# Kernel tuning notes

Measured on AMD Instinct MI355X. Metric: run time of the kernel, lower is better.

The kernel has to match this reference:

```python
import jax, jax.numpy as jnp
import numpy as np

L = 43          # number of classes
C = L + 3       # <eps>, 'O', 'I-', + L class symbols
B = 128
T = 4096
NEG = jnp.float32(-1e30)


def setup_inputs() -> dict:
    key = jax.random.key(0)
    k1, k2, k3, k4 = jax.random.split(key, 4)
    logits = jax.random.normal(k1, (B, T, C), dtype=jnp.float32)
    log_probs = jax.nn.log_softmax(logits, axis=-1)
    input_lens = jax.random.randint(k2, (B,), T // 2, T + 1).astype(jnp.int32)
    labels = jax.random.randint(k3, (B, T), 1, C).astype(jnp.int32)  # valid (non-eps) symbols
    # den_scores parameter: one raw score per denominator arc (2L+4 arcs).
    # Layout: [0]=0->0 'O', [1:L+1]=0->0 labels, [L+1]=0->1 'I-', [L+2]=0->final,
    #         [L+3]=1->1 'I-', [L+4:2L+4]=1->0 labels.
    den_params = 0.01 * jax.random.normal(k4, (2 * L + 4,), dtype=jnp.float32)
    return {"log_probs": log_probs, "den_params": den_params,
            "input_lens": input_lens, "labels": labels}


def reference(log_probs, den_params, input_lens, labels):
    Bb, Tt, Cc = log_probs.shape
    Ll = Cc - 3
    # set_scores_stochastic_: per-source-state log-softmax of arc scores
    g0 = jax.nn.log_softmax(den_params[: Ll + 3])   # state-0 outgoing arcs
    g1 = jax.nn.log_softmax(den_params[Ll + 3:])    # state-1 outgoing arcs
    s_O, s0_lab, s_0I, s_fin = g0[0], g0[1:Ll + 1], g0[Ll + 1], g0[Ll + 2]
    s_1I, s1_lab = g1[0], g1[1:]

    mask = jnp.arange(Tt)[None, :] < input_lens[:, None]          # [B,T]

    # ---- numerator: linear FSA intersected with emissions = path score ----
    tok_lp = jnp.take_along_axis(log_probs, labels[..., None], axis=-1)[..., 0]
    num = jnp.sum(jnp.where(mask, tok_lp, 0.0), axis=1)           # [B]

    # ---- denominator: log-semiring forward DP over the 2-state topology ----
    lp_t = jnp.moveaxis(log_probs, 1, 0)    # [T,B,C]
    mask_t = jnp.moveaxis(mask, 1, 0)       # [T,B]

    def step(alpha, inputs):
        lp, m = inputs                       # lp [B,C], m [B]
        a0, a1 = alpha[:, 0], alpha[:, 1]
        lp_lab = lp[:, 3:]                   # emissions for class symbols, [B,L]
        # into state 0: 0->0 on 'O', 0->0 on each label, 1->0 on each label
        terms0 = jnp.concatenate([
            (a0 + s_O + lp[:, 1])[:, None],
            a0[:, None] + s0_lab[None, :] + lp_lab,
            a1[:, None] + s1_lab[None, :] + lp_lab,
        ], axis=1)
        n0 = jax.scipy.special.logsumexp(terms0, axis=1)
        # into state 1: 0->1 and 1->1, both on 'I-'
        terms1 = jnp.stack([a0 + s_0I + lp[:, 2], a1 + s_1I + lp[:, 2]], axis=1)
        n1 = jax.scipy.special.logsumexp(terms1, axis=1)
        new = jnp.stack([n0, n1], axis=1)
        new = jnp.where(m[:, None], new, alpha)  # frozen past each seq's length
        return new, None

    alpha0 = jnp.concatenate(
        [jnp.zeros((Bb, 1), log_probs.dtype), jnp.full((Bb, 1), NEG, log_probs.dtype)], axis=1)
    alpha, _ = jax.lax.scan(step, alpha0, (lp_t, mask_t))
    den = alpha[:, 0] + s_fin                                    # final arc 0->2 on -1

    return jnp.sum(num - den)
```

## Files before the change

kernel.cpp:

```cpp
#include <hip/hip_runtime.h>

#define BB 128
#define TT 4096
#define LL 43
#define CC 46
#define CHUNK 256
#define NC (TT / CHUNK)
#define TPB 256
#define NEGF (-1e30f)
#define L2E 1.44269504088896340736f
#define LN2 0.69314718055994530942f

__device__ __forceinline__ float la2(float x, float y) {
    float mx = fmaxf(x, y), mn = fminf(x, y);
    return mx + log2f(1.0f + exp2f(mn - mx));
}

__global__ void crf_prep(const float* __restrict__ dp, float* __restrict__ cst) {
    int lane = threadIdx.x;
    float x0 = (lane < CC) ? dp[lane] : NEGF;
    float x1 = (lane < LL + 1) ? dp[CC + lane] : NEGF;
    float mx0 = x0, mx1 = x1;
    #pragma unroll
    for (int m = 1; m < 64; m <<= 1) {
        mx0 = fmaxf(mx0, __shfl_xor(mx0, m));
        mx1 = fmaxf(mx1, __shfl_xor(mx1, m));
    }
    float e0 = (lane < CC) ? expf(x0 - mx0) : 0.0f;
    float e1 = (lane < LL + 1) ? expf(x1 - mx1) : 0.0f;
    float s0 = e0, s1 = e1;
    #pragma unroll
    for (int m = 1; m < 64; m <<= 1) {
        s0 += __shfl_xor(s0, m);
        s1 += __shfl_xor(s1, m);
    }
    float g0 = x0 - mx0 - logf(s0);
    float g1 = x1 - mx1 - logf(s1);
    if (lane >= 1 && lane <= LL) {
        cst[lane - 1] = expf(g0);
        cst[LL + lane - 1] = expf(g1);
    }
    if (lane == 0) { cst[86] = expf(g0); cst[88] = g1 * L2E; }
    if (lane == LL + 1) cst[87] = g0 * L2E;
    if (lane == LL + 2) cst[89] = g0 * L2E;
}

__global__ __launch_bounds__(TPB) void crf_chunk(
    const float* __restrict__ lp, const int* __restrict__ lens,
    const int* __restrict__ labels, const float* __restrict__ cst,
    float* __restrict__ res) {
    int b = blockIdx.y, c = blockIdx.x;
    int t0 = c * CHUNK;
    int len = lens[b];
    float* r = res + (b * NC + c) * 8;
    if (t0 >= len) {
        if (threadIdx.x == 0) { r[0] = 0.f; r[1] = NEGF; r[2] = NEGF; r[3] = 0.f; r[4] = 0.f; }
        return;
    }
    __shared__ float tile[CHUNK * CC];
    __shared__ float wres[TPB / 64][5];
    const float4* src = (const float4*)(lp + (size_t)(b * TT + t0) * CC);
    float4* dst = (float4*)tile;
    #pragma unroll 4
    for (int i = threadIdx.x; i < CHUNK * CC / 4; i += TPB) dst[i] = src[i];
    __syncthreads();

    int tid = threadIdx.x;
    int t = t0 + tid;
    const float* vr = tile + tid * CC;
    float m00, m01, m10, m11, tok;
    {
        float w1 = exp2f(L2E * vr[1]);
        float v2s = L2E * vr[2];
        float dot0 = cst[2 * LL] * w1;
        float dot1 = 0.f;
        #pragma unroll
        for (int j = 0; j < LL; ++j) {
            float w = exp2f(L2E * vr[3 + j]);
            dot0 = fmaf(cst[j], w, dot0);
            dot1 = fmaf(cst[LL + j], w, dot1);
        }
        m00 = log2f(dot0);
        m01 = log2f(dot1);
        m10 = cst[87] + v2s;
        m11 = cst[88] + v2s;
        int lab = labels[b * TT + t];
        tok = vr[lab];
    }
    if (t >= len) { m00 = 0.f; m01 = NEGF; m10 = NEGF; m11 = 0.f; tok = 0.f; }

    int lane = tid & 63;
    #pragma unroll
    for (int m = 1; m < 64; m <<= 1) {
        float p00 = __shfl_xor(m00, m), p01 = __shfl_xor(m01, m);
        float p10 = __shfl_xor(m10, m), p11 = __shfl_xor(m11, m);
        bool up = (lane & m) != 0;
        float a00 = up ? m00 : p00, a01 = up ? m01 : p01;
        float a10 = up ? m10 : p10, a11 = up ? m11 : p11;
        float b00 = up ? p00 : m00, b01 = up ? p01 : m01;
        float b10 = up ? p10 : m10, b11 = up ? p11 : m11;
        m00 = la2(a00 + b00, a01 + b10);
        m01 = la2(a00 + b01, a01 + b11);
        m10 = la2(a10 + b00, a11 + b10);
        m11 = la2(a10 + b01, a11 + b11);
        tok += __shfl_xor(tok, m);
    }
    if (lane == 0) {
        int w = tid >> 6;
        wres[w][0] = m00; wres[w][1] = m01; wres[w][2] = m10; wres[w][3] = m11; wres[w][4] = tok;
    }
    __syncthreads();
    if (tid == 0) {
        float c00 = wres[0][0], c01 = wres[0][1], c10 = wres[0][2], c11 = wres[0][3];
        float num = wres[0][4];
        #pragma unroll
        for (int w = 1; w < TPB / 64; ++w) {
            float a00 = wres[w][0], a01 = wres[w][1], a10 = wres[w][2], a11 = wres[w][3];
            float n00 = la2(a00 + c00, a01 + c10);
            float n01 = la2(a00 + c01, a01 + c11);
            float n10 = la2(a10 + c00, a11 + c10);
            float n11 = la2(a10 + c01, a11 + c11);
            c00 = n00; c01 = n01; c10 = n10; c11 = n11;
            num += wres[w][4];
        }
        r[0] = c00; r[1] = c01; r[2] = c10; r[3] = c11; r[4] = num;
    }
}

__global__ void crf_final(const float* __restrict__ cst, const float* __restrict__ res,
                          float* __restrict__ out) {
    int b = threadIdx.x;
    float a0 = 0.f, a1 = NEGF, num = 0.f;
    #pragma unroll
    for (int c = 0; c < NC; ++c) {
        const float* r = res + (b * NC + c) * 8;
        float n0 = la2(r[0] + a0, r[1] + a1);
        float n1 = la2(r[2] + a0, r[3] + a1);
        a0 = n0; a1 = n1; num += r[4];
    }
    float den = (a0 + cst[89]) * LN2;
    float val = num - den;
    #pragma unroll
    for (int m = 1; m < 64; m <<= 1) val += __shfl_xor(val, m);
    __shared__ float part[2];
    if ((b & 63) == 0) part[b >> 6] = val;
    __syncthreads();
    if (b == 0) out[0] = part[0] + part[1];
}

extern "C" void kernel_launch(void* const* d_in, const int* in_sizes, int n_in,
                              void* d_out, int out_size, void* d_ws, size_t ws_size,
                              hipStream_t stream) {
    const float* lp = (const float*)d_in[0];
    const float* dp = (const float*)d_in[1];
    const int* lens = (const int*)d_in[2];
    const int* labels = (const int*)d_in[3];
    float* out = (float*)d_out;
    float* cst = (float*)d_ws;
    float* res = cst + 96;

    hipLaunchKernelGGL(crf_prep, dim3(1), dim3(64), 0, stream, dp, cst);
    hipLaunchKernelGGL(crf_chunk, dim3(NC, BB), dim3(TPB), 0, stream, lp, lens, labels, cst, res);
    hipLaunchKernelGGL(crf_final, dim3(1), dim3(128), 0, stream, cst, res, out);
}
```

Before: 157.4 us.

## Fuse prep, chunk and final kernels into one with last-block reduction

Merges the three launches into a single kernel. Each block recomputes the softmaxed arc scores into shared memory, and the last block to finish, found through an atomic counter, runs the final cross-chunk combine and batch sum. Emission reads are widened to float2 and the label load is issued before the tile copy. This removes two kernel launches and the global constant round trip. In exchange every block does redundant prep work, masked blocks now sync and take part in the counter, and an extra memset launch is added.

```diff
diff --git a/kernel.cpp b/kernel.cpp
--- a/kernel.cpp
+++ b/kernel.cpp
@@ -7,6 +7,7 @@
 #define CHUNK 256
 #define NC (TT / CHUNK)
 #define TPB 256
+#define NBLK (NC * BB)
 #define NEGF (-1e30f)
 #define L2E 1.44269504088896340736f
 #define LN2 0.69314718055994530942f
@@ -16,75 +17,89 @@
     return mx + log2f(1.0f + exp2f(mn - mx));
 }
 
-__global__ void crf_prep(const float* __restrict__ dp, float* __restrict__ cst) {
-    int lane = threadIdx.x;
-    float x0 = (lane < CC) ? dp[lane] : NEGF;
-    float x1 = (lane < LL + 1) ? dp[CC + lane] : NEGF;
-    float mx0 = x0, mx1 = x1;
-    #pragma unroll
-    for (int m = 1; m < 64; m <<= 1) {
-        mx0 = fmaxf(mx0, __shfl_xor(mx0, m));
-        mx1 = fmaxf(mx1, __shfl_xor(mx1, m));
-    }
-    float e0 = (lane < CC) ? expf(x0 - mx0) : 0.0f;
-    float e1 = (lane < LL + 1) ? expf(x1 - mx1) : 0.0f;
-    float s0 = e0, s1 = e1;
-    #pragma unroll
-    for (int m = 1; m < 64; m <<= 1) {
-        s0 += __shfl_xor(s0, m);
-        s1 += __shfl_xor(s1, m);
-    }
-    float g0 = x0 - mx0 - logf(s0);
-    float g1 = x1 - mx1 - logf(s1);
-    if (lane >= 1 && lane <= LL) {
-        cst[lane - 1] = expf(g0);
-        cst[LL + lane - 1] = expf(g1);
-    }
-    if (lane == 0) { cst[86] = expf(g0); cst[88] = g1 * L2E; }
-    if (lane == LL + 1) cst[87] = g0 * L2E;
-    if (lane == LL + 2) cst[89] = g0 * L2E;
-}
+__global__ __launch_bounds__(TPB) void crf_fused(
+    const float* __restrict__ lp, const float* __restrict__ dp,
+    const int* __restrict__ lens, const int* __restrict__ labels,
+    float* __restrict__ res, unsigned* __restrict__ cnt,
+    float* __restrict__ out) {
+    __shared__ float tile[CHUNK * CC];
+    __shared__ float2 pp[LL];
+    __shared__ float sc[4];
+    __shared__ float wres[TPB / 64][5];
+    __shared__ float part[4];
+    __shared__ int flagsh;
 
-__global__ __launch_bounds__(TPB) void crf_chunk(
-    const float* __restrict__ lp, const int* __restrict__ lens,
-    const int* __restrict__ labels, const float* __restrict__ cst,
-    float* __restrict__ res) {
     int b = blockIdx.y, c = blockIdx.x;
     int t0 = c * CHUNK;
     int len = lens[b];
-    float* r = res + (b * NC + c) * 8;
-    if (t0 >= len) {
-        if (threadIdx.x == 0) { r[0] = 0.f; r[1] = NEGF; r[2] = NEGF; r[3] = 0.f; r[4] = 0.f; }
-        return;
+    bool masked = (t0 >= len);
+    int tid = threadIdx.x;
+
+    if (tid < 64) {
+        int lane = tid;
+        float x0 = (lane < CC) ? dp[lane] : NEGF;
+        float x1 = (lane < LL + 1) ? dp[CC + lane] : NEGF;
+        float mx0 = x0, mx1 = x1;
+        #pragma unroll
+        for (int m = 1; m < 64; m <<= 1) {
+            mx0 = fmaxf(mx0, __shfl_xor(mx0, m));
+            mx1 = fmaxf(mx1, __shfl_xor(mx1, m));
+        }
+        float e0 = (lane < CC) ? expf(x0 - mx0) : 0.0f;
+        float e1 = (lane < LL + 1) ? expf(x1 - mx1) : 0.0f;
+        float s0 = e0, s1 = e1;
+        #pragma unroll
+        for (int m = 1; m < 64; m <<= 1) {
+            s0 += __shfl_xor(s0, m);
+            s1 += __shfl_xor(s1, m);
+        }
+        float g0 = x0 - mx0 - logf(s0);
+        float g1 = x1 - mx1 - logf(s1);
+        if (lane >= 1 && lane <= LL) { pp[lane - 1].x = expf(g0); pp[lane - 1].y = expf(g1); }
+        if (lane == 0) { sc[0] = expf(g0); sc[2] = g1 * L2E; }
+        if (lane == LL + 1) sc[1] = g0 * L2E;
+        if (lane == LL + 2) sc[3] = g0 * L2E;
     }
-    __shared__ float tile[CHUNK * CC];
-    __shared__ float wres[TPB / 64][5];
-    const float4* src = (const float4*)(lp + (size_t)(b * TT + t0) * CC);
-    float4* dst = (float4*)tile;
-    #pragma unroll 4
-    for (int i = threadIdx.x; i < CHUNK * CC / 4; i += TPB) dst[i] = src[i];
+
+    int t = t0 + tid;
+    int lab = labels[b * TT + t];
+
+    if (!masked) {
+        const float4* src = (const float4*)(lp + (size_t)(b * TT + t0) * CC);
+        float4* dst = (float4*)tile;
+        #pragma unroll 4
+        for (int i = tid; i < CHUNK * CC / 4; i += TPB) dst[i] = src[i];
+    }
     __syncthreads();
 
-    int tid = threadIdx.x;
-    int t = t0 + tid;
     const float* vr = tile + tid * CC;
     float m00, m01, m10, m11, tok;
     {
-        float w1 = exp2f(L2E * vr[1]);
-        float v2s = L2E * vr[2];
-        float dot0 = cst[2 * LL] * w1;
+        const float2* vr2 = (const float2*)vr;
+        float2 c01 = vr2[0];
+        float2 c23 = vr2[1];
+        float w1 = exp2f(L2E * c01.y);
+        float v2s = L2E * c23.x;
+        float dot0 = sc[0] * w1;
         float dot1 = 0.f;
+        {
+            float w = exp2f(L2E * c23.y);
+            float2 p = pp[0];
+            dot0 = fmaf(p.x, w, dot0);
+            dot1 = fmaf(p.y, w, dot1);
+        }
         #pragma unroll
-        for (int j = 0; j < LL; ++j) {
-            float w = exp2f(L2E * vr[3 + j]);
-            dot0 = fmaf(cst[j], w, dot0);
-            dot1 = fmaf(cst[LL + j], w, dot1);
+        for (int k = 2; k <= 22; ++k) {
+            float2 v = vr2[k];
+            float wa = exp2f(L2E * v.x), wb = exp2f(L2E * v.y);
+            float2 pa = pp[2 * k - 3], pb = pp[2 * k - 2];
+            dot0 = fmaf(pa.x, wa, dot0); dot1 = fmaf(pa.y, wa, dot1);
+            dot0 = fmaf(pb.x, wb, dot0); dot1 = fmaf(pb.y, wb, dot1);
         }
         m00 = log2f(dot0);
         m01 = log2f(dot1);
-        m10 = cst[87] + v2s;
-        m11 = cst[88] + v2s;
-        int lab = labels[b * TT + t];
+        m10 = sc[1] + v2s;
+        m11 = sc[2] + v2s;
         tok = vr[lab];
     }
     if (t >= len) { m00 = 0.f; m01 = NEGF; m10 = NEGF; m11 = 0.f; tok = 0.f; }
@@ -110,6 +125,7 @@
         wres[w][0] = m00; wres[w][1] = m01; wres[w][2] = m10; wres[w][3] = m11; wres[w][4] = tok;
     }
     __syncthreads();
+
     if (tid == 0) {
         float c00 = wres[0][0], c01 = wres[0][1], c10 = wres[0][2], c11 = wres[0][3];
         float num = wres[0][4];
@@ -123,29 +139,43 @@
             c00 = n00; c01 = n01; c10 = n10; c11 = n11;
             num += wres[w][4];
         }
-        r[0] = c00; r[1] = c01; r[2] = c10; r[3] = c11; r[4] = num;
+        float* r = res + (b * NC + c) * 8;
+        __hip_atomic_store(r + 0, c00, __ATOMIC_RELAXED, __HIP_MEMORY_SCOPE_AGENT);
+        __hip_atomic_store(r + 1, c01, __ATOMIC_RELAXED, __HIP_MEMORY_SCOPE_AGENT);
+        __hip_atomic_store(r + 2, c10, __ATOMIC_RELAXED, __HIP_MEMORY_SCOPE_AGENT);
+        __hip_atomic_store(r + 3, c11, __ATOMIC_RELAXED, __HIP_MEMORY_SCOPE_AGENT);
+        __hip_atomic_store(r + 4, num, __ATOMIC_RELAXED, __HIP_MEMORY_SCOPE_AGENT);
+        __threadfence();
+        unsigned old = __hip_atomic_fetch_add(cnt, 1u, __ATOMIC_ACQ_REL, __HIP_MEMORY_SCOPE_AGENT);
+        flagsh = (old == NBLK - 1) ? 1 : 0;
     }
-}
+    __syncthreads();
 
-__global__ void crf_final(const float* __restrict__ cst, const float* __restrict__ res,
-                          float* __restrict__ out) {
-    int b = threadIdx.x;
-    float a0 = 0.f, a1 = NEGF, num = 0.f;
-    #pragma unroll
-    for (int c = 0; c < NC; ++c) {
-        const float* r = res + (b * NC + c) * 8;
-        float n0 = la2(r[0] + a0, r[1] + a1);
-        float n1 = la2(r[2] + a0, r[3] + a1);
-        a0 = n0; a1 = n1; num += r[4];
+    if (flagsh) {
+        __threadfence();
+        float val = 0.f;
+        if (tid < BB) {
+            float a0 = 0.f, a1 = NEGF, num = 0.f;
+            #pragma unroll 4
+            for (int cc = 0; cc < NC; ++cc) {
+                const float* r = res + (tid * NC + cc) * 8;
+                float r0 = __hip_atomic_load(r + 0, __ATOMIC_RELAXED, __HIP_MEMORY_SCOPE_AGENT);
+                float r1 = __hip_atomic_load(r + 1, __ATOMIC_RELAXED, __HIP_MEMORY_SCOPE_AGENT);
+                float r2 = __hip_atomic_load(r + 2, __ATOMIC_RELAXED, __HIP_MEMORY_SCOPE_AGENT);
+                float r3 = __hip_atomic_load(r + 3, __ATOMIC_RELAXED, __HIP_MEMORY_SCOPE_AGENT);
+                float r4 = __hip_atomic_load(r + 4, __ATOMIC_RELAXED, __HIP_MEMORY_SCOPE_AGENT);
+                float n0 = la2(r0 + a0, r1 + a1);
+                float n1 = la2(r2 + a0, r3 + a1);
+                a0 = n0; a1 = n1; num += r4;
+            }
+            val = num - (a0 + sc[3]) * LN2;
+        }
+        #pragma unroll
+        for (int m = 1; m < 64; m <<= 1) val += __shfl_xor(val, m);
+        if ((tid & 63) == 0) part[tid >> 6] = val;
+        __syncthreads();
+        if (tid == 0) out[0] = part[0] + part[1] + part[2] + part[3];
     }
-    float den = (a0 + cst[89]) * LN2;
-    float val = num - den;
-    #pragma unroll
-    for (int m = 1; m < 64; m <<= 1) val += __shfl_xor(val, m);
-    __shared__ float part[2];
-    if ((b & 63) == 0) part[b >> 6] = val;
-    __syncthreads();
-    if (b == 0) out[0] = part[0] + part[1];
 }
 
 extern "C" void kernel_launch(void* const* d_in, const int* in_sizes, int n_in,
@@ -156,10 +186,10 @@
     const int* lens = (const int*)d_in[2];
     const int* labels = (const int*)d_in[3];
     float* out = (float*)d_out;
-    float* cst = (float*)d_ws;
-    float* res = cst + 96;
+    float* res = (float*)d_ws;
+    unsigned* cnt = (unsigned*)((char*)d_ws + 65536);
 
-    hipLaunchKernelGGL(crf_prep, dim3(1), dim3(64), 0, stream, dp, cst);
-    hipLaunchKernelGGL(crf_chunk, dim3(NC, BB), dim3(TPB), 0, stream, lp, lens, labels, cst, res);
-    hipLaunchKernelGGL(crf_final, dim3(1), dim3(128), 0, stream, cst, res, out);
+    hipMemsetAsync(cnt, 0, sizeof(unsigned), stream);
+    hipLaunchKernelGGL(crf_fused, dim3(NC, BB), dim3(TPB), 0, stream,
+                       lp, dp, lens, labels, res, cnt, out);
 }
```

After: 274.5 us. 1.74x slower.
